# Kernel tuning notes

Hardware: AMD Instinct MI355X
Metric: run time of the kernel (lower is better)

Reference implementation:

```python
import jax, jax.numpy as jnp
import numpy as np

HIDDEN = 256
DEPTH = 3
MOL_ATOMS = 42  # padding_final_size in MPNEncoder.padding (AM_dim0=False)
ATOM_FDIM = 133
BOND_FDIM = 147
N_MOLS = 4000
N_ATOMS = N_MOLS * MOL_ATOMS
N_BONDS = 360000
MAX_NB = 6


def setup_inputs() -> dict:
    key = jax.random.key(0)
    ks = jax.random.split(key, 9)
    f_atoms = jax.random.normal(ks[0], (N_ATOMS, ATOM_FDIM), dtype=jnp.float32)
    f_bonds = jax.random.normal(ks[1], (N_BONDS, BOND_FDIM), dtype=jnp.float32)
    a2b = jax.random.randint(ks[2], (N_ATOMS, MAX_NB), 0, N_BONDS, dtype=jnp.int32)
    b2a = jax.random.randint(ks[3], (N_BONDS,), 0, N_ATOMS, dtype=jnp.int32)
    b2revb = jax.random.randint(ks[4], (N_BONDS,), 0, N_BONDS, dtype=jnp.int32)
    # learned params (bias=False for W_i/W_h, W_o has bias, per chemprop defaults)
    W_i = jax.random.normal(ks[5], (HIDDEN, BOND_FDIM), dtype=jnp.float32) * 0.05
    W_h = jax.random.normal(ks[6], (HIDDEN, HIDDEN), dtype=jnp.float32) * 0.05
    W_o = jax.random.normal(ks[7], (HIDDEN, ATOM_FDIM + HIDDEN), dtype=jnp.float32) * 0.05
    b_o = jax.random.normal(ks[8], (HIDDEN,), dtype=jnp.float32) * 0.05
    return dict(f_atoms=f_atoms, f_bonds=f_bonds, W_i=W_i, W_h=W_h, W_o=W_o,
                b_o=b_o, a2b=a2b, b2a=b2a, b2revb=b2revb)


def reference(f_atoms, f_bonds, W_i, W_h, W_o, b_o, a2b, b2a, b2revb):
    # bond-message MPN (atom_messages=False, undirected=False, dropout=0)
    relu = jax.nn.relu
    inp = f_bonds @ W_i.T                         # [n_bonds, H]
    message = relu(inp)

    def atom_hidden(a_msg):
        a_input = jnp.concatenate([f_atoms, a_msg], axis=1)  # [n_atoms, fa+H]
        return relu(a_input @ W_o.T + b_o)

    # depth-0 hidden: a_input = [f_atoms, zeros(H)] (the 'padding' tensor)
    save_depth = [atom_hidden(jnp.zeros((f_atoms.shape[0], HIDDEN), f_atoms.dtype))]
    for d in range(DEPTH - 1):
        if d == 0:
            save_depth.append(atom_hidden(message[a2b].sum(axis=1)))
        a_message = message[a2b].sum(axis=1)      # gather+sum over neighbors
        message = a_message[b2a] - message[b2revb]
        message = relu(inp + message @ W_h.T)
        save_depth.append(atom_hidden(message[a2b].sum(axis=1)))

    # every molecule has exactly MOL_ATOMS atoms -> padding() is identity,
    # per-molecule narrow/stack becomes a reshape
    def pool(h):
        return h.reshape(N_MOLS, MOL_ATOMS, HIDDEN)

    d0, d1, d2 = pool(save_depth[0]), pool(save_depth[1]), pool(save_depth[2])
    dfin = pool(save_depth[-1])
    mol_vecs = dfin.mean(axis=1)                  # sum / a_size
    return (d0, d1, d2, dfin, mol_vecs)
```

## Files before the change

kernel.cpp:

```cpp
#include <hip/hip_runtime.h>

typedef unsigned short u16;
typedef unsigned int u32;
typedef __bf16 bf16x8 __attribute__((ext_vector_type(8)));
typedef float f32x4 __attribute__((ext_vector_type(4)));

__device__ __forceinline__ u16 f2bf(float f) {
  union { float f; u32 u; } c; c.f = f;
  return (u16)((c.u + 0x7fffu + ((c.u >> 16) & 1u)) >> 16);
}
__device__ __forceinline__ float bf2f(u16 h) {
  union { u32 u; float f; } c; c.u = ((u32)h) << 16;
  return c.f;
}
__device__ __forceinline__ float bflo(u32 u) {
  union { u32 u; float f; } c; c.u = u << 16; return c.f;
}
__device__ __forceinline__ float bfhi(u32 u) {
  union { u32 u; float f; } c; c.u = u & 0xffff0000u; return c.f;
}

__global__ __launch_bounds__(256) void cvt_w(const float* __restrict__ src,
                                             u16* __restrict__ dst, int N,
                                             int Ks, int Kd, int src_stride,
                                             int col0) {
  int i = blockIdx.x * 256 + threadIdx.x;
  if (i >= N * Kd) return;
  int n = i / Kd, k = i % Kd;
  float v = (k < Ks) ? src[(size_t)n * src_stride + col0 + k] : 0.f;
  dst[i] = f2bf(v);
}

template <int ASRC, int EPI, int KPAD>
__global__ __launch_bounds__(256, 3) void gemm2(
    const float* __restrict__ Af, int lda, int Kreal,
    const u16* __restrict__ Ab, const u16* __restrict__ Ab2,
    const int* __restrict__ idx1, const int* __restrict__ idx2,
    const u16* __restrict__ Bw,
    const u16* __restrict__ addb, const float* __restrict__ bias,
    u16* __restrict__ outb0, u16* __restrict__ outb1,
    float* __restrict__ outf) {
  constexpr int LDK = KPAD + 8;
  __shared__ u16 As[64 * LDK];

  const int tid = threadIdx.x;
  const int lane = tid & 63, wid = tid >> 6;
  const int wn = wid * 64;
  const int m0 = blockIdx.x * 64;

  if (ASRC == 2) {
    const int r = tid >> 2, part = tid & 3;
    const int gr = m0 + r;
    const int r1 = idx1[gr], r2 = idx2[gr];
    const u16* pa = Ab + (size_t)r1 * KPAD + part * (KPAD / 4);
    const u16* pb = Ab2 + (size_t)r2 * KPAD + part * (KPAD / 4);
    u16* dst = &As[r * LDK + part * (KPAD / 4)];
#pragma unroll
    for (int i = 0; i < KPAD / 32; ++i) {
      uint4 va = *reinterpret_cast<const uint4*>(pa + i * 8);
      uint4 vb = *reinterpret_cast<const uint4*>(pb + i * 8);
      uint4 v;
      u16 t0, t1;
      t0 = f2bf(bflo(va.x) - bflo(vb.x));
      t1 = f2bf(bfhi(va.x) - bfhi(vb.x));
      v.x = (u32)t0 | ((u32)t1 << 16);
      t0 = f2bf(bflo(va.y) - bflo(vb.y));
      t1 = f2bf(bfhi(va.y) - bfhi(vb.y));
      v.y = (u32)t0 | ((u32)t1 << 16);
      t0 = f2bf(bflo(va.z) - bflo(vb.z));
      t1 = f2bf(bfhi(va.z) - bfhi(vb.z));
      v.z = (u32)t0 | ((u32)t1 << 16);
      t0 = f2bf(bflo(va.w) - bflo(vb.w));
      t1 = f2bf(bfhi(va.w) - bfhi(vb.w));
      v.w = (u32)t0 | ((u32)t1 << 16);
      *reinterpret_cast<uint4*>(dst + i * 8) = v;
    }
  } else if (ASRC == 1) {
    constexpr int NCH = 64 * KPAD / 8;
#pragma unroll
    for (int p = 0; p < NCH / 256; ++p) {
      int ch = p * 256 + tid;
      int row = ch / (KPAD / 8);
      int c8 = ch % (KPAD / 8);
      uint4 v = *reinterpret_cast<const uint4*>(Ab + (size_t)m0 * KPAD + (size_t)ch * 8);
      *reinterpret_cast<uint4*>(&As[row * LDK + c8 * 8]) = v;
    }
  } else {
    constexpr int NE = 64 * KPAD;
#pragma unroll
    for (int p = 0; p < NE / 256; ++p) {
      int e = p * 256 + tid;
      int row = e / KPAD, k = e % KPAD;
      float x = (k < Kreal) ? Af[(size_t)(m0 + row) * lda + k] : 0.f;
      As[row * LDK + k] = f2bf(x);
    }
  }
  __syncthreads();

  f32x4 acc[4][4];
#pragma unroll
  for (int i = 0; i < 4; ++i)
#pragma unroll
    for (int j = 0; j < 4; ++j) acc[i][j] = (f32x4)(0.f);

  const int ar = lane & 15, ak = (lane >> 4) * 8;

#pragma unroll
  for (int kk = 0; kk < KPAD; kk += 32) {
    bf16x8 a[4], b[4];
#pragma unroll
    for (int t = 0; t < 4; ++t)
      a[t] = *reinterpret_cast<const bf16x8*>(&As[(t * 16 + ar) * LDK + kk + ak]);
#pragma unroll
    for (int t = 0; t < 4; ++t)
      b[t] = *reinterpret_cast<const bf16x8*>(Bw + (size_t)(wn + t * 16 + ar) * KPAD + kk + ak);
#pragma unroll
    for (int i = 0; i < 4; ++i)
#pragma unroll
      for (int j = 0; j < 4; ++j)
        acc[i][j] = __builtin_amdgcn_mfma_f32_16x16x32_bf16(a[i], b[j], acc[i][j], 0, 0, 0);
  }

  const int er = (lane >> 4) * 4;
  const int ec = lane & 15;
#pragma unroll
  for (int i = 0; i < 4; ++i) {
#pragma unroll
    for (int j = 0; j < 4; ++j) {
      int rbase = m0 + i * 16 + er;
      int c = wn + j * 16 + ec;
#pragma unroll
      for (int q = 0; q < 4; ++q) {
        int r = rbase + q;
        size_t idx = (size_t)r * 256 + c;
        float v = acc[i][j][q];
        if (EPI == 0) {
          outb0[idx] = f2bf(v);
          outb1[idx] = f2bf(v > 0.f ? v : 0.f);
        } else if (EPI == 1) {
          v += bias[c];
          outb0[idx] = f2bf(v);
          outf[idx] = v > 0.f ? v : 0.f;
        } else if (EPI == 2) {
          v += bf2f(addb[idx]);
          outb1[idx] = f2bf(v > 0.f ? v : 0.f);
        } else {
          v += bf2f(addb[idx]);
          outf[idx] = v > 0.f ? v : 0.f;
        }
      }
    }
  }
}

__global__ __launch_bounds__(256) void gather_sum(const u16* __restrict__ msg,
                                                  const int* __restrict__ a2b,
                                                  u16* __restrict__ amsg,
                                                  int n_atoms) {
  int wave = threadIdx.x >> 6, lane = threadIdx.x & 63;
  int atom = blockIdx.x * 4 + wave;
  if (atom >= n_atoms) return;
  float s0 = 0.f, s1 = 0.f, s2 = 0.f, s3 = 0.f;
  int base = atom * 6;
#pragma unroll
  for (int j = 0; j < 6; ++j) {
    int b = a2b[base + j];
    ushort4 v = *reinterpret_cast<const ushort4*>(msg + (size_t)b * 256 + lane * 4);
    s0 += bf2f(v.x);
    s1 += bf2f(v.y);
    s2 += bf2f(v.z);
    s3 += bf2f(v.w);
  }
  ushort4 o = make_ushort4(f2bf(s0), f2bf(s1), f2bf(s2), f2bf(s3));
  *reinterpret_cast<ushort4*>(amsg + (size_t)atom * 256 + lane * 4) = o;
}

__global__ __launch_bounds__(256) void mol_mean(const float* __restrict__ dfin,
                                                float* __restrict__ out) {
  int mol = blockIdx.x, c = threadIdx.x;
  const float* p = dfin + (size_t)mol * (42 * 256) + c;
  float s = 0.f;
#pragma unroll
  for (int a = 0; a < 42; ++a) s += p[a * 256];
  out[(size_t)mol * 256 + c] = s * (1.0f / 42.0f);
}

extern "C" void kernel_launch(void* const* d_in, const int* in_sizes, int n_in,
                              void* d_out, int out_size, void* d_ws,
                              size_t ws_size, hipStream_t stream) {
  const float* f_atoms = (const float*)d_in[0];
  const float* f_bonds = (const float*)d_in[1];
  const float* W_i = (const float*)d_in[2];
  const float* W_h = (const float*)d_in[3];
  const float* W_o = (const float*)d_in[4];
  const float* b_o = (const float*)d_in[5];
  const int* a2b = (const int*)d_in[6];
  const int* b2a = (const int*)d_in[7];
  const int* b2revb = (const int*)d_in[8];

  const int NA = 168000, NB = 360000, H = 256;
  const size_t SZ_BH = (size_t)NB * H * 2;
  const size_t SZ_AH = (size_t)NA * H * 2;

  char* ws = (char*)d_ws;
  u16* inp_b = (u16*)ws;  ws += SZ_BH;
  u16* msgA  = (u16*)ws;  ws += SZ_BH;
  u16* msgB  = (u16*)ws;  ws += SZ_BH;
  u16* amsg  = (u16*)ws;  ws += SZ_AH;
  u16* base_b = (u16*)ws; ws += SZ_AH;
  u16* Wi_b  = (u16*)ws;  ws += 256 * 192 * 2;
  u16* Wh_b  = (u16*)ws;  ws += 256 * 256 * 2;
  u16* Wo1_b = (u16*)ws;  ws += 256 * 192 * 2;
  u16* Wo2_b = (u16*)ws;  ws += 256 * 256 * 2;

  float* out = (float*)d_out;
  float* d0 = out;
  float* d1 = d0 + (size_t)NA * H;
  float* d2 = d1 + (size_t)NA * H;
  float* dfin = d2 + (size_t)NA * H;
  float* mol = dfin + (size_t)NA * H;

  dim3 blk(256);
  cvt_w<<<dim3((256 * 192 + 255) / 256), blk, 0, stream>>>(W_i, Wi_b, 256, 147, 192, 147, 0);
  cvt_w<<<dim3((256 * 256 + 255) / 256), blk, 0, stream>>>(W_h, Wh_b, 256, 256, 256, 256, 0);
  cvt_w<<<dim3((256 * 192 + 255) / 256), blk, 0, stream>>>(W_o, Wo1_b, 256, 133, 192, 389, 0);
  cvt_w<<<dim3((256 * 256 + 255) / 256), blk, 0, stream>>>(W_o, Wo2_b, 256, 256, 256, 389, 133);

  dim3 gB(NB / 64);
  dim3 gA(NA / 64);

  gemm2<0, 0, 192><<<gB, blk, 0, stream>>>(f_bonds, 147, 147, nullptr, nullptr,
                                           nullptr, nullptr, Wi_b, nullptr,
                                           nullptr, inp_b, msgA, nullptr);
  gemm2<0, 1, 192><<<gA, blk, 0, stream>>>(f_atoms, 133, 133, nullptr, nullptr,
                                           nullptr, nullptr, Wo1_b, nullptr,
                                           b_o, base_b, nullptr, d0);

  u16* mcur = msgA;
  u16* mnext = msgB;
  float* douts[3] = {d1, d2, dfin};
  for (int d = 0; d < 3; ++d) {
    gather_sum<<<dim3(NA / 4), blk, 0, stream>>>(mcur, a2b, amsg, NA);
    gemm2<1, 3, 256><<<gA, blk, 0, stream>>>(nullptr, 0, 0, amsg, nullptr,
                                             nullptr, nullptr, Wo2_b, base_b,
                                             nullptr, nullptr, nullptr, douts[d]);
    if (d < 2) {
      gemm2<2, 2, 256><<<gB, blk, 0, stream>>>(nullptr, 0, 0, amsg, mcur, b2a,
                                               b2revb, Wh_b, inp_b, nullptr,
                                               nullptr, mnext, nullptr);
      u16* t = mcur; mcur = mnext; mnext = t;
    }
  }
  mol_mean<<<dim3(4000), blk, 0, stream>>>(dfin, mol);
}
```

Before: 1.755 ms.

## Rewrite GEMMs as LDS-free 32-row tiles and store pre-ReLU messages

Replaces the shared-memory GEMM with a kernel that loads A fragments straight from global memory into MFMA operands, using 32-row tiles and K padded to 160 instead of 192. The bond buffers now hold pre-activation values, and ReLU is applied when they are read in gather_sum and in a new bond_sub kernel. That kernel does the b2a/b2revb gather-subtract on its own, which takes the indexed gather out of the GEMM. Epilogue stores become vectorised and the initial GEMM writes one output instead of two. In exchange, the subtract result now makes an extra round trip through memory and the A loads from global are uncoalesced.

```diff
diff --git a/kernel.cpp b/kernel.cpp
--- a/kernel.cpp
+++ b/kernel.cpp
@@ -5,19 +5,21 @@
 typedef __bf16 bf16x8 __attribute__((ext_vector_type(8)));
 typedef float f32x4 __attribute__((ext_vector_type(4)));
 
-__device__ __forceinline__ u16 f2bf(float f) {
-  union { float f; u32 u; } c; c.f = f;
-  return (u16)((c.u + 0x7fffu + ((c.u >> 16) & 1u)) >> 16);
-}
 __device__ __forceinline__ float bf2f(u16 h) {
-  union { u32 u; float f; } c; c.u = ((u32)h) << 16;
-  return c.f;
+  union { u32 u; float f; } c; c.u = ((u32)h) << 16; return c.f;
 }
 __device__ __forceinline__ float bflo(u32 u) {
   union { u32 u; float f; } c; c.u = u << 16; return c.f;
 }
 __device__ __forceinline__ float bfhi(u32 u) {
   union { u32 u; float f; } c; c.u = u & 0xffff0000u; return c.f;
+}
+__device__ __forceinline__ u32 pack2bf(float a, float b) {
+  union { __bf16 h[2]; u32 u; } c; c.h[0] = (__bf16)a; c.h[1] = (__bf16)b;
+  return c.u;
+}
+__device__ __forceinline__ u16 f2bf(float f) {
+  union { __bf16 h; u16 u; } c; c.h = (__bf16)f; return c.u;
 }
 
 __global__ __launch_bounds__(256) void cvt_w(const float* __restrict__ src,
@@ -32,128 +34,99 @@
 }
 
 template <int ASRC, int EPI, int KPAD>
-__global__ __launch_bounds__(256, 3) void gemm2(
-    const float* __restrict__ Af, int lda, int Kreal,
-    const u16* __restrict__ Ab, const u16* __restrict__ Ab2,
-    const int* __restrict__ idx1, const int* __restrict__ idx2,
-    const u16* __restrict__ Bw,
+__global__ __launch_bounds__(256, 3) void gemm4(
+    const float* __restrict__ Af, int Kreal,
+    const u16* __restrict__ Ab, const u16* __restrict__ Bw,
     const u16* __restrict__ addb, const float* __restrict__ bias,
-    u16* __restrict__ outb0, u16* __restrict__ outb1,
-    float* __restrict__ outf) {
-  constexpr int LDK = KPAD + 8;
-  __shared__ u16 As[64 * LDK];
-
+    u16* __restrict__ outb0, float* __restrict__ outf) {
   const int tid = threadIdx.x;
-  const int lane = tid & 63, wid = tid >> 6;
-  const int wn = wid * 64;
-  const int m0 = blockIdx.x * 64;
-
-  if (ASRC == 2) {
-    const int r = tid >> 2, part = tid & 3;
-    const int gr = m0 + r;
-    const int r1 = idx1[gr], r2 = idx2[gr];
-    const u16* pa = Ab + (size_t)r1 * KPAD + part * (KPAD / 4);
-    const u16* pb = Ab2 + (size_t)r2 * KPAD + part * (KPAD / 4);
-    u16* dst = &As[r * LDK + part * (KPAD / 4)];
-#pragma unroll
-    for (int i = 0; i < KPAD / 32; ++i) {
-      uint4 va = *reinterpret_cast<const uint4*>(pa + i * 8);
-      uint4 vb = *reinterpret_cast<const uint4*>(pb + i * 8);
-      uint4 v;
-      u16 t0, t1;
-      t0 = f2bf(bflo(va.x) - bflo(vb.x));
-      t1 = f2bf(bfhi(va.x) - bfhi(vb.x));
-      v.x = (u32)t0 | ((u32)t1 << 16);
-      t0 = f2bf(bflo(va.y) - bflo(vb.y));
-      t1 = f2bf(bfhi(va.y) - bfhi(vb.y));
-      v.y = (u32)t0 | ((u32)t1 << 16);
-      t0 = f2bf(bflo(va.z) - bflo(vb.z));
-      t1 = f2bf(bfhi(va.z) - bfhi(vb.z));
-      v.z = (u32)t0 | ((u32)t1 << 16);
-      t0 = f2bf(bflo(va.w) - bflo(vb.w));
-      t1 = f2bf(bfhi(va.w) - bfhi(vb.w));
-      v.w = (u32)t0 | ((u32)t1 << 16);
-      *reinterpret_cast<uint4*>(dst + i * 8) = v;
-    }
-  } else if (ASRC == 1) {
-    constexpr int NCH = 64 * KPAD / 8;
-#pragma unroll
-    for (int p = 0; p < NCH / 256; ++p) {
-      int ch = p * 256 + tid;
-      int row = ch / (KPAD / 8);
-      int c8 = ch % (KPAD / 8);
-      uint4 v = *reinterpret_cast<const uint4*>(Ab + (size_t)m0 * KPAD + (size_t)ch * 8);
-      *reinterpret_cast<uint4*>(&As[row * LDK + c8 * 8]) = v;
-    }
-  } else {
-    constexpr int NE = 64 * KPAD;
-#pragma unroll
-    for (int p = 0; p < NE / 256; ++p) {
-      int e = p * 256 + tid;
-      int row = e / KPAD, k = e % KPAD;
-      float x = (k < Kreal) ? Af[(size_t)(m0 + row) * lda + k] : 0.f;
-      As[row * LDK + k] = f2bf(x);
-    }
-  }
-  __syncthreads();
-
-  f32x4 acc[4][4];
-#pragma unroll
-  for (int i = 0; i < 4; ++i)
+  const int lane = tid & 63;
+  const int wn = (tid >> 6) * 64;
+  const int m0 = blockIdx.x * 32;
+  const int lm = lane & 15, lg = lane >> 4;
+  const int koff = lg * 8;
+
+  f32x4 acc[2][4];
+#pragma unroll
+  for (int i = 0; i < 2; ++i)
 #pragma unroll
     for (int j = 0; j < 4; ++j) acc[i][j] = (f32x4)(0.f);
 
-  const int ar = lane & 15, ak = (lane >> 4) * 8;
-
-#pragma unroll
-  for (int kk = 0; kk < KPAD; kk += 32) {
-    bf16x8 a[4], b[4];
-#pragma unroll
-    for (int t = 0; t < 4; ++t)
-      a[t] = *reinterpret_cast<const bf16x8*>(&As[(t * 16 + ar) * LDK + kk + ak]);
-#pragma unroll
-    for (int t = 0; t < 4; ++t)
-      b[t] = *reinterpret_cast<const bf16x8*>(Bw + (size_t)(wn + t * 16 + ar) * KPAD + kk + ak);
-#pragma unroll
-    for (int i = 0; i < 4; ++i)
-#pragma unroll
-      for (int j = 0; j < 4; ++j)
-        acc[i][j] = __builtin_amdgcn_mfma_f32_16x16x32_bf16(a[i], b[j], acc[i][j], 0, 0, 0);
-  }
-
-  const int er = (lane >> 4) * 4;
-  const int ec = lane & 15;
-#pragma unroll
-  for (int i = 0; i < 4; ++i) {
-#pragma unroll
-    for (int j = 0; j < 4; ++j) {
-      int rbase = m0 + i * 16 + er;
-      int c = wn + j * 16 + ec;
-#pragma unroll
-      for (int q = 0; q < 4; ++q) {
-        int r = rbase + q;
-        size_t idx = (size_t)r * 256 + c;
-        float v = acc[i][j][q];
-        if (EPI == 0) {
-          outb0[idx] = f2bf(v);
-          outb1[idx] = f2bf(v > 0.f ? v : 0.f);
-        } else if (EPI == 1) {
-          v += bias[c];
-          outb0[idx] = f2bf(v);
-          outf[idx] = v > 0.f ? v : 0.f;
-        } else if (EPI == 2) {
-          v += bf2f(addb[idx]);
-          outb1[idx] = f2bf(v > 0.f ? v : 0.f);
+#pragma unroll
+  for (int kk = 0; kk < KPAD / 32; ++kk) {
+    const int k0 = kk * 32 + koff;
+    bf16x8 a[2];
+#pragma unroll
+    for (int im = 0; im < 2; ++im) {
+      if constexpr (ASRC == 0) {
+        const float* p = Af + (size_t)(m0 + im * 16 + lm) * Kreal + k0;
+        union { bf16x8 v; u32 u[4]; } cv;
+        if (k0 + 8 <= Kreal) {
+#pragma unroll
+          for (int e = 0; e < 4; ++e) cv.u[e] = pack2bf(p[2 * e], p[2 * e + 1]);
         } else {
-          v += bf2f(addb[idx]);
-          outf[idx] = v > 0.f ? v : 0.f;
+#pragma unroll
+          for (int e = 0; e < 4; ++e) {
+            float x0 = (k0 + 2 * e < Kreal) ? p[2 * e] : 0.f;
+            float x1 = (k0 + 2 * e + 1 < Kreal) ? p[2 * e + 1] : 0.f;
+            cv.u[e] = pack2bf(x0, x1);
+          }
         }
+        a[im] = cv.v;
+      } else {
+        a[im] = *reinterpret_cast<const bf16x8*>(
+            Ab + (size_t)(m0 + im * 16 + lm) * KPAD + k0);
       }
     }
-  }
-}
-
-__global__ __launch_bounds__(256) void gather_sum(const u16* __restrict__ msg,
+#pragma unroll
+    for (int jw = 0; jw < 4; ++jw) {
+      bf16x8 b = *reinterpret_cast<const bf16x8*>(
+          Bw + (size_t)(wn + jw * 16 + lm) * KPAD + k0);
+      acc[0][jw] = __builtin_amdgcn_mfma_f32_16x16x32_bf16(b, a[0], acc[0][jw], 0, 0, 0);
+      acc[1][jw] = __builtin_amdgcn_mfma_f32_16x16x32_bf16(b, a[1], acc[1][jw], 0, 0, 0);
+    }
+  }
+
+#pragma unroll
+  for (int im = 0; im < 2; ++im) {
+#pragma unroll
+    for (int jw = 0; jw < 4; ++jw) {
+      const int r = m0 + im * 16 + lm;
+      const int c0 = wn + jw * 16 + lg * 4;
+      const size_t idx = (size_t)r * 256 + c0;
+      f32x4 v = acc[im][jw];
+      if constexpr (EPI == 0) {
+        uint2 o; o.x = pack2bf(v[0], v[1]); o.y = pack2bf(v[2], v[3]);
+        *reinterpret_cast<uint2*>(outb0 + idx) = o;
+      } else if constexpr (EPI == 1) {
+        const float4 bb = *reinterpret_cast<const float4*>(bias + c0);
+        v[0] += bb.x; v[1] += bb.y; v[2] += bb.z; v[3] += bb.w;
+        uint2 o; o.x = pack2bf(v[0], v[1]); o.y = pack2bf(v[2], v[3]);
+        *reinterpret_cast<uint2*>(outb0 + idx) = o;
+        float4 rl;
+        rl.x = v[0] > 0.f ? v[0] : 0.f; rl.y = v[1] > 0.f ? v[1] : 0.f;
+        rl.z = v[2] > 0.f ? v[2] : 0.f; rl.w = v[3] > 0.f ? v[3] : 0.f;
+        *reinterpret_cast<float4*>(outf + idx) = rl;
+      } else if constexpr (EPI == 2) {
+        const uint2 ab = *reinterpret_cast<const uint2*>(addb + idx);
+        v[0] += bflo(ab.x); v[1] += bfhi(ab.x);
+        v[2] += bflo(ab.y); v[3] += bfhi(ab.y);
+        uint2 o; o.x = pack2bf(v[0], v[1]); o.y = pack2bf(v[2], v[3]);
+        *reinterpret_cast<uint2*>(outb0 + idx) = o;
+      } else {
+        const uint2 ab = *reinterpret_cast<const uint2*>(addb + idx);
+        v[0] += bflo(ab.x); v[1] += bfhi(ab.x);
+        v[2] += bflo(ab.y); v[3] += bfhi(ab.y);
+        float4 rl;
+        rl.x = v[0] > 0.f ? v[0] : 0.f; rl.y = v[1] > 0.f ? v[1] : 0.f;
+        rl.z = v[2] > 0.f ? v[2] : 0.f; rl.w = v[3] > 0.f ? v[3] : 0.f;
+        *reinterpret_cast<float4*>(outf + idx) = rl;
+      }
+    }
+  }
+}
+
+__global__ __launch_bounds__(256) void gather_sum(const u16* __restrict__ S,
                                                   const int* __restrict__ a2b,
                                                   u16* __restrict__ amsg,
                                                   int n_atoms) {
@@ -165,14 +138,38 @@
 #pragma unroll
   for (int j = 0; j < 6; ++j) {
     int b = a2b[base + j];
-    ushort4 v = *reinterpret_cast<const ushort4*>(msg + (size_t)b * 256 + lane * 4);
-    s0 += bf2f(v.x);
-    s1 += bf2f(v.y);
-    s2 += bf2f(v.z);
-    s3 += bf2f(v.w);
-  }
-  ushort4 o = make_ushort4(f2bf(s0), f2bf(s1), f2bf(s2), f2bf(s3));
-  *reinterpret_cast<ushort4*>(amsg + (size_t)atom * 256 + lane * 4) = o;
+    ushort4 v = *reinterpret_cast<const ushort4*>(S + (size_t)b * 256 + lane * 4);
+    float x;
+    x = bf2f(v.x); s0 += x > 0.f ? x : 0.f;
+    x = bf2f(v.y); s1 += x > 0.f ? x : 0.f;
+    x = bf2f(v.z); s2 += x > 0.f ? x : 0.f;
+    x = bf2f(v.w); s3 += x > 0.f ? x : 0.f;
+  }
+  uint2 o;
+  o.x = pack2bf(s0, s1);
+  o.y = pack2bf(s2, s3);
+  *reinterpret_cast<uint2*>(amsg + (size_t)atom * 256 + lane * 4) = o;
+}
+
+__global__ __launch_bounds__(256) void bond_sub(const u16* __restrict__ amsg,
+                                                const u16* __restrict__ S,
+                                                const int* __restrict__ b2a,
+                                                const int* __restrict__ b2revb,
+                                                u16* __restrict__ pm, int nb) {
+  int wave = threadIdx.x >> 6, lane = threadIdx.x & 63;
+  int b = blockIdx.x * 4 + wave;
+  if (b >= nb) return;
+  int r1 = b2a[b], r2 = b2revb[b];
+  uint2 va = *reinterpret_cast<const uint2*>(amsg + (size_t)r1 * 256 + lane * 4);
+  uint2 vb = *reinterpret_cast<const uint2*>(S + (size_t)r2 * 256 + lane * 4);
+  float a0 = bflo(va.x), a1 = bfhi(va.x), a2 = bflo(va.y), a3 = bfhi(va.y);
+  float b0 = bflo(vb.x), b1 = bfhi(vb.x), b2 = bflo(vb.y), b3 = bfhi(vb.y);
+  b0 = b0 > 0.f ? b0 : 0.f; b1 = b1 > 0.f ? b1 : 0.f;
+  b2 = b2 > 0.f ? b2 : 0.f; b3 = b3 > 0.f ? b3 : 0.f;
+  uint2 o;
+  o.x = pack2bf(a0 - b0, a1 - b1);
+  o.y = pack2bf(a2 - b2, a3 - b3);
+  *reinterpret_cast<uint2*>(pm + (size_t)b * 256 + lane * 4) = o;
 }
 
 __global__ __launch_bounds__(256) void mol_mean(const float* __restrict__ dfin,
@@ -204,13 +201,13 @@
 
   char* ws = (char*)d_ws;
   u16* inp_b = (u16*)ws;  ws += SZ_BH;
-  u16* msgA  = (u16*)ws;  ws += SZ_BH;
-  u16* msgB  = (u16*)ws;  ws += SZ_BH;
+  u16* P0    = (u16*)ws;  ws += SZ_BH;
+  u16* P1    = (u16*)ws;  ws += SZ_BH;
   u16* amsg  = (u16*)ws;  ws += SZ_AH;
   u16* base_b = (u16*)ws; ws += SZ_AH;
-  u16* Wi_b  = (u16*)ws;  ws += 256 * 192 * 2;
+  u16* Wi_b  = (u16*)ws;  ws += 256 * 160 * 2;
   u16* Wh_b  = (u16*)ws;  ws += 256 * 256 * 2;
-  u16* Wo1_b = (u16*)ws;  ws += 256 * 192 * 2;
+  u16* Wo1_b = (u16*)ws;  ws += 256 * 160 * 2;
   u16* Wo2_b = (u16*)ws;  ws += 256 * 256 * 2;
 
   float* out = (float*)d_out;
@@ -221,34 +218,27 @@
   float* mol = dfin + (size_t)NA * H;
 
   dim3 blk(256);
-  cvt_w<<<dim3((256 * 192 + 255) / 256), blk, 0, stream>>>(W_i, Wi_b, 256, 147, 192, 147, 0);
+  cvt_w<<<dim3((256 * 160 + 255) / 256), blk, 0, stream>>>(W_i, Wi_b, 256, 147, 160, 147, 0);
   cvt_w<<<dim3((256 * 256 + 255) / 256), blk, 0, stream>>>(W_h, Wh_b, 256, 256, 256, 256, 0);
-  cvt_w<<<dim3((256 * 192 + 255) / 256), blk, 0, stream>>>(W_o, Wo1_b, 256, 133, 192, 389, 0);
+  cvt_w<<<dim3((256 * 160 + 255) / 256), blk, 0, stream>>>(W_o, Wo1_b, 256, 133, 160, 389, 0);
   cvt_w<<<dim3((256 * 256 + 255) / 256), blk, 0, stream>>>(W_o, Wo2_b, 256, 256, 256, 389, 133);
 
-  dim3 gB(NB / 64);
-  dim3 gA(NA / 64);
-
-  gemm2<0, 0, 192><<<gB, blk, 0, stream>>>(f_bonds, 147, 147, nullptr, nullptr,
-                                           nullptr, nullptr, Wi_b, nullptr,
-                                           nullptr, inp_b, msgA, nullptr);
-  gemm2<0, 1, 192><<<gA, blk, 0, stream>>>(f_atoms, 133, 133, nullptr, nullptr,
-                                           nullptr, nullptr, Wo1_b, nullptr,
-                                           b_o, base_b, nullptr, d0);
-
-  u16* mcur = msgA;
-  u16* mnext = msgB;
+  gemm4<0, 0, 160><<<dim3(NB / 32), blk, 0, stream>>>(
+      f_bonds, 147, nullptr, Wi_b, nullptr, nullptr, inp_b, nullptr);
+  gemm4<0, 1, 160><<<dim3(NA / 32), blk, 0, stream>>>(
+      f_atoms, 133, nullptr, Wo1_b, nullptr, b_o, base_b, d0);
+
+  u16* S = inp_b;
   float* douts[3] = {d1, d2, dfin};
   for (int d = 0; d < 3; ++d) {
-    gather_sum<<<dim3(NA / 4), blk, 0, stream>>>(mcur, a2b, amsg, NA);
-    gemm2<1, 3, 256><<<gA, blk, 0, stream>>>(nullptr, 0, 0, amsg, nullptr,
-                                             nullptr, nullptr, Wo2_b, base_b,
-                                             nullptr, nullptr, nullptr, douts[d]);
+    gather_sum<<<dim3(NA / 4), blk, 0, stream>>>(S, a2b, amsg, NA);
+    gemm4<1, 3, 256><<<dim3(NA / 32), blk, 0, stream>>>(
+        nullptr, 0, amsg, Wo2_b, base_b, nullptr, nullptr, douts[d]);
     if (d < 2) {
-      gemm2<2, 2, 256><<<gB, blk, 0, stream>>>(nullptr, 0, 0, amsg, mcur, b2a,
-                                               b2revb, Wh_b, inp_b, nullptr,
-                                               nullptr, mnext, nullptr);
-      u16* t = mcur; mcur = mnext; mnext = t;
+      bond_sub<<<dim3(NB / 4), blk, 0, stream>>>(amsg, S, b2a, b2revb, P0, NB);
+      gemm4<1, 2, 256><<<dim3(NB / 32), blk, 0, stream>>>(
+          nullptr, 0, P0, Wh_b, inp_b, nullptr, P1, nullptr);
+      S = P1;
     }
   }
   mol_mean<<<dim3(4000), blk, 0, stream>>>(dfin, mol);
```

New measurement: 2.065 ms. 17.7% more time.
